# Optimization experiments

Hardware: AMD Instinct MI355X
Metric: run time of the kernel (lower is better)

The kernel has to match this reference:

```python
import math
import jax, jax.numpy as jnp
import numpy as np

C, H, W = 128, 64, 64
R, K = 7, 3          # 7x3 dilated window
PAD_H, PAD_W = 9, 2  # from unfold paddings
DIL_H, DIL_W = 3, 2  # row/col dilations


def _neighborhood(x):
    """Gather dilated 7x3 neighborhood: out[n,c,r,k,i,j] = x[n,c, i+3r-9, j+2k-2] (zero-padded).
    x: (n,c,h,w) -> (n,c,7,3,h,w)."""
    n, c, h, w = x.shape
    xp = jnp.pad(x, ((0, 0), (0, 0), (PAD_H, PAD_H), (PAD_W, PAD_W)))
    taps = [xp[:, :, DIL_H * r:DIL_H * r + h, DIL_W * k:DIL_W * k + w]
            for r in range(R) for k in range(K)]
    return jnp.stack(taps, axis=2).reshape(n, c, R, K, h, w)


def setup_inputs() -> dict:
    key = jax.random.key(0)
    k1, k2, k3 = jax.random.split(key, 3)
    x = jax.random.normal(k1, (4, C, H, W), dtype=jnp.float32)
    p5_w = 0.1 * jax.random.normal(k2, (1, C, R, K, H, W), dtype=jnp.float32)
    p6_w = 0.1 * jax.random.normal(k3, (1, C, R, K, C), dtype=jnp.float32)
    return {"x": x, "p5_w": p5_w, "p6_w": p6_w}


def reference(x, p5_w, p6_w):
    n, c, h, w = x.shape
    # t_2: dilated 7x3 neighborhood gather (double unfold)
    t2 = _neighborhood(x)                                   # (n,c,7,3,h,w)
    # t_3: bmm((n,c*21,hw), (n,hw,c)) / sqrt(hw)
    t3 = jnp.einsum('ncrkhw,ndhw->ncrkd', t2, x) / math.sqrt(h * w)  # (n,c,7,3,c)
    # elementwise modulation
    t7 = p5_w * t2 + t2                                     # (n,c,7,3,h,w)
    t6 = p6_w * t3                                          # (n,c,7,3,c)
    # t_8: bmm((n,hw,c*21), (n,c*21,c)) / sqrt(c*21)
    t8 = jnp.einsum('ncrkhw,ncrkd->nhwd', t7, t6) / math.sqrt(c * R * K)  # (n,h,w,c)
    return jnp.transpose(t8, (0, 3, 1, 2))                  # (n,c,h,w)
```

## Files before the change

### kernel.cpp

```cpp
#include <hip/hip_runtime.h>

typedef _Float16 f16;
typedef _Float16 f16x2 __attribute__((ext_vector_type(2)));
typedef _Float16 f16x4 __attribute__((ext_vector_type(4)));
typedef _Float16 f16x8 __attribute__((ext_vector_type(8)));
typedef float    f32x4 __attribute__((ext_vector_type(4)));

#define XROWS 82
#define XSTR  (XROWS * 64)
#define XK_ELEMS (3u * 4u * 128u * (unsigned)XSTR)
static const size_t T6T_OFF   = (size_t)XK_ELEMS * 2;
static const size_t T6T_BYTES = (size_t)4 * 128 * 2688 * 2;
static const size_t T3P_OFF   = T6T_OFF + T6T_BYTES;
static const size_t T8P_OFF   = T3P_OFF;

__device__ __forceinline__ void gl16(const f16* g, f16* l) {
  __builtin_amdgcn_global_load_lds((const __attribute__((address_space(1))) void*)g,
                                   (__attribute__((address_space(3))) void*)l, 16, 0, 0);
}

__global__ __launch_bounds__(256) void prep_kernel(const float* __restrict__ x,
                                                   f16* __restrict__ xk) {
  unsigned p = blockIdx.x * 256u + threadIdx.x;
  unsigned total = 3u * 4u * 128u * 82u * 32u;
  if (p >= total) return;
  unsigned wp   = p & 31u;
  unsigned row  = (p >> 5) % 82u;
  unsigned rest = p / (32u * 82u);
  unsigned c    = rest & 127u;
  unsigned rest2 = rest >> 7;
  unsigned n    = rest2 & 3u;
  unsigned kc   = rest2 >> 2;
  int hsrc = (int)row - 9;
  int wsrc = (int)(wp * 2u) + 2 * (int)kc - 2;
  f16x2 v; v.x = (f16)0.f; v.y = (f16)0.f;
  if (hsrc >= 0 && hsrc < 64 && wsrc >= 0 && wsrc < 64) {
    const float2* src = (const float2*)(x + (((size_t)(n * 128u + c) * 64u + (unsigned)hsrc) * 64u + (unsigned)wsrc));
    float2 xv = *src;
    v.x = (f16)(xv.x * 0.125f);
    v.y = (f16)(xv.y * 0.125f);
  }
  ((f16x2*)xk)[p] = v;
}

__global__ __launch_bounds__(256, 3) void gram_kernel(const f16* __restrict__ xk,
                                                      f16* __restrict__ t3p) {
  __shared__ f16 gl[2 * 12288];

  unsigned b    = blockIdx.x;
  unsigned ks   = b & 7u;
  unsigned cseg = (b >> 3) & 1u;
  unsigned rki  = (b >> 4) % 11u;
  unsigned n    = b / 176u;
  unsigned r    = rki / 3u;
  unsigned kc   = rki - r * 3u;

  unsigned tid  = threadIdx.x;
  unsigned wv   = tid >> 6;
  unsigned lane = tid & 63u;
  unsigned wy   = wv >> 1;
  unsigned wx   = wv & 1u;
  unsigned quad = lane >> 4;
  unsigned l16  = lane & 15u;
  unsigned rsl  = lane >> 3;
  unsigned seg  = (lane & 7u) ^ (rsl & 7u);

  unsigned h0 = ks * 8u;
  const f16* Ab = xk + (size_t)(kc * 4u + n) * 128u * XSTR + (size_t)(cseg * 64u) * XSTR
                + (h0 + 3u * r) * 64u + seg * 8u;
  const f16* Bb = xk + (size_t)(4u + n) * 128u * XSTR + (h0 + 9u) * 64u + seg * 8u;
  unsigned ar0 = wv * 16u;
  unsigned br0 = wv * 32u;

  f32x4 acc[2][4] = {};

#pragma unroll
  for (unsigned t = 0; t < 2u; t++)
    gl16(Ab + (size_t)(ar0 + t * 8u + rsl) * XSTR, &gl[(ar0 + t * 8u) * 64u]);
#pragma unroll
  for (unsigned t = 0; t < 4u; t++)
    gl16(Bb + (size_t)(br0 + t * 8u + rsl) * XSTR, &gl[4096u + (br0 + t * 8u) * 64u]);

  for (unsigned s = 0; s < 8u; s++) {
    __syncthreads();
    if (s < 7u) {
      f16* base = &gl[((s + 1u) & 1u) * 12288u];
      unsigned off = (s + 1u) * 64u;
#pragma unroll
      for (unsigned t = 0; t < 2u; t++)
        gl16(Ab + off + (size_t)(ar0 + t * 8u + rsl) * XSTR, base + (ar0 + t * 8u) * 64u);
#pragma unroll
      for (unsigned t = 0; t < 4u; t++)
        gl16(Bb + off + (size_t)(br0 + t * 8u + rsl) * XSTR, base + 4096u + (br0 + t * 8u) * 64u);
    }
    const f16* bufA = &gl[(s & 1u) * 12288u];
    const f16* bufB = bufA + 4096u;
#pragma unroll
    for (unsigned t2 = 0; t2 < 2u; t2++) {
      unsigned L = t2 * 4u + quad;
      f16x8 a[2], bb[4];
#pragma unroll
      for (int ms = 0; ms < 2; ms++) {
        unsigned rr = wy * 32u + (unsigned)ms * 16u + l16;
        a[ms] = *(const f16x8*)&bufA[rr * 64u + (L ^ (rr & 7u)) * 8u];
      }
#pragma unroll
      for (int ns = 0; ns < 4; ns++) {
        unsigned rb = wx * 64u + (unsigned)ns * 16u + l16;
        bb[ns] = *(const f16x8*)&bufB[rb * 64u + (L ^ (rb & 7u)) * 8u];
      }
#pragma unroll
      for (int ms = 0; ms < 2; ms++)
#pragma unroll
        for (int ns = 0; ns < 4; ns++)
          acc[ms][ns] = __builtin_amdgcn_mfma_f32_16x16x32_f16(a[ms], bb[ns], acc[ms][ns], 0, 0, 0);
    }
  }

  f16* tp = t3p + ((size_t)(ks * 4u + n) * 11u + rki) * 16384u;
#pragma unroll
  for (int ms = 0; ms < 2; ms++) {
#pragma unroll
    for (int ns = 0; ns < 4; ns++) {
      unsigned c0 = cseg * 64u + wy * 32u + (unsigned)ms * 16u + quad * 4u;
      unsigned d  = wx * 64u + (unsigned)ns * 16u + l16;
#pragma unroll
      for (int reg = 0; reg < 4; reg++)
        tp[(size_t)(c0 + (unsigned)reg) * 128u + d] = (f16)acc[ms][ns][reg];
    }
  }
}

__global__ __launch_bounds__(256) void ep_kernel(const f16* __restrict__ t3p,
                                                 const float* __restrict__ p6,
                                                 f16* __restrict__ t6T) {
  unsigned idx = blockIdx.x * 256u + threadIdx.x;
  unsigned t   = idx >> 12;
  unsigned rk  = t % 21u;
  unsigned n   = t / 21u;

  if (rk <= 10u) {
    unsigned d4 = idx & 31u;
    unsigned c  = (idx >> 5) & 127u;
    unsigned d0 = d4 * 4u;
    float s0 = 0.f, s1 = 0.f, s2 = 0.f, s3 = 0.f;
#pragma unroll
    for (unsigned ks = 0; ks < 8u; ks++) {
      f16x4 v = *(const f16x4*)(t3p + (((size_t)(ks * 4u + n) * 11u + rk) * 16384u + c * 128u + d0));
      s0 += (float)v[0]; s1 += (float)v[1]; s2 += (float)v[2]; s3 += (float)v[3];
    }
    const float* pp = p6 + ((size_t)c * 21u + rk) * 128u + d0;
    f16* ob = t6T + (size_t)(n * 128u + d0) * 2688u + rk * 128u + c;
    ob[0]        = (f16)(s0 * pp[0]);
    ob[2688]     = (f16)(s1 * pp[1]);
    ob[2 * 2688] = (f16)(s2 * pp[2]);
    ob[3 * 2688] = (f16)(s3 * pp[3]);
  } else {
    unsigned mrk = 20u - rk;
    unsigned c4 = idx & 31u;
    unsigned d  = (idx >> 5) & 127u;
    unsigned c0 = c4 * 4u;
    float s0 = 0.f, s1 = 0.f, s2 = 0.f, s3 = 0.f;
#pragma unroll
    for (unsigned ks = 0; ks < 8u; ks++) {
      f16x4 v = *(const f16x4*)(t3p + (((size_t)(ks * 4u + n) * 11u + mrk) * 16384u + d * 128u + c0));
      s0 += (float)v[0]; s1 += (float)v[1]; s2 += (float)v[2]; s3 += (float)v[3];
    }
    f16x4 o;
    o[0] = (f16)(s0 * p6[((size_t)(c0 + 0u) * 21u + rk) * 128u + d]);
    o[1] = (f16)(s1 * p6[((size_t)(c0 + 1u) * 21u + rk) * 128u + d]);
    o[2] = (f16)(s2 * p6[((size_t)(c0 + 2u) * 21u + rk) * 128u + d]);
    o[3] = (f16)(s3 * p6[((size_t)(c0 + 3u) * 21u + rk) * 128u + d]);
    *(f16x4*)(t6T + (size_t)(n * 128u + d) * 2688u + rk * 128u + c0) = o;
  }
}

#define ALDS_STR 40
#define RT_STR   66
__global__ __launch_bounds__(256, 4) void outp_kernel(const f16* __restrict__ xk,
                                                      const float* __restrict__ p5,
                                                      const f16* __restrict__ t6T,
                                                      f16* __restrict__ t8p) {
  __shared__ float smem[8448];
  f16* Alds = (f16*)smem;

  unsigned b = blockIdx.x;
  unsigned g = b & 3u;
  unsigned h = (b >> 2) & 63u;
  unsigned n = b >> 8;

  unsigned tid  = threadIdx.x;
  unsigned wv   = tid >> 6;
  unsigned lane = tid & 63u;
  unsigned wy   = wv >> 1;
  unsigned wx   = wv & 1u;
  unsigned quad = lane >> 4;
  unsigned l16  = lane & 15u;
  unsigned wst  = tid & 63u;
  unsigned g8   = tid >> 6;

  unsigned cbase = g * 32u + g8 * 8u;
  const float* prow0 = p5 + (size_t)cbase * (21u * 4096u) + h * 64u + wst;
  const f16* bfb = t6T + (size_t)(n * 128u + wx * 64u + l16) * 2688u + g * 32u + quad * 8u;

  f32x4 acc[2][4] = {};
  f16 xv[8]; float pv[8];
  f16x8 bfc[4];

  {
    const f16* xrow = xk + (((size_t)n * 128u + cbase) * XROWS + h) * 64u + wst;
#pragma unroll
    for (int i = 0; i < 8; i++) { xv[i] = xrow[(size_t)i * XSTR]; pv[i] = prow0[(size_t)i * (21u * 4096u)]; }
#pragma unroll
    for (int ns = 0; ns < 4; ns++) bfc[ns] = *(const f16x8*)(bfb + (size_t)ns * 16u * 2688u);
  }

  for (unsigned j = 0; j < 21u; j++) {
    f16* Ag = Alds + (j & 1u) * 2560u;
    {
      f16x8 av;
#pragma unroll
      for (int i = 0; i < 8; i++) av[i] = (f16)((float)xv[i] * (1.0f + pv[i]));
      *(f16x8*)&Ag[wst * ALDS_STR + g8 * 8u] = av;
    }
    __syncthreads();

    f16x8 bfn[4];
    if (j < 20u) {
      unsigned rk = j + 1u;
      unsigned rr = rk / 3u;
      unsigned kcc = rk - rr * 3u;
      const f16* xrow = xk + (((size_t)(kcc * 4u + n) * 128u + cbase) * XROWS + (h + 3u * rr)) * 64u + wst;
      const float* prow = prow0 + rk * 4096u;
#pragma unroll
      for (int i = 0; i < 8; i++) { xv[i] = xrow[(size_t)i * XSTR]; pv[i] = prow[(size_t)i * (21u * 4096u)]; }
#pragma unroll
      for (int ns = 0; ns < 4; ns++) bfn[ns] = *(const f16x8*)(bfb + (size_t)ns * 16u * 2688u + rk * 128u);
    }

    f16x8 a[2];
#pragma unroll
    for (int ms = 0; ms < 2; ms++)
      a[ms] = *(const f16x8*)&Ag[(wy * 32u + (unsigned)ms * 16u + l16) * ALDS_STR + quad * 8u];
#pragma unroll
    for (int ms = 0; ms < 2; ms++)
#pragma unroll
      for (int ns = 0; ns < 4; ns++)
        acc[ms][ns] = __builtin_amdgcn_mfma_f32_16x16x32_f16(a[ms], bfc[ns], acc[ms][ns], 0, 0, 0);
#pragma unroll
    for (int ns = 0; ns < 4; ns++) bfc[ns] = bfn[ns];
  }

  __syncthreads();
  float* Rt = smem;
#pragma unroll
  for (int ms = 0; ms < 2; ms++)
#pragma unroll
    for (int ns = 0; ns < 4; ns++) {
      unsigned w0 = wy * 32u + (unsigned)ms * 16u + quad * 4u;
      unsigned d  = wx * 64u + (unsigned)ns * 16u + l16;
#pragma unroll
      for (int reg = 0; reg < 4; reg++)
        Rt[d * RT_STR + w0 + (unsigned)reg] = acc[ms][ns][reg];
    }
  __syncthreads();
  f16* op = t8p + ((size_t)((g * 4u + n) * 64u + h)) * 8192u;
#pragma unroll
  for (unsigned it = 0; it < 4u; it++) {
    unsigned row = (tid >> 3) + it * 32u;
    unsigned w0  = (tid & 7u) * 8u;
    f16x8 o;
#pragma unroll
    for (int i = 0; i < 8; i++) o[i] = (f16)Rt[row * RT_STR + w0 + (unsigned)i];
    *(f16x8*)(op + row * 64u + w0) = o;
  }
}

__global__ __launch_bounds__(256) void red_kernel(const f16* __restrict__ t8p,
                                                  float* __restrict__ out) {
  unsigned idx = blockIdx.x * 256u + threadIdx.x;
  unsigned w0 = (idx & 7u) * 8u;
  unsigned h  = (idx >> 3) & 63u;
  unsigned d  = (idx >> 9) & 127u;
  unsigned n  = idx >> 16;
  const float FS = 0.15430334996209192f;
  float s[8] = {};
#pragma unroll
  for (unsigned g = 0; g < 4u; g++) {
    f16x8 v = *(const f16x8*)(t8p + ((size_t)((g * 4u + n) * 64u + h)) * 8192u + d * 64u + w0);
#pragma unroll
    for (int i = 0; i < 8; i++) s[i] += (float)v[i];
  }
  f32x4 o0, o1;
#pragma unroll
  for (int i = 0; i < 4; i++) { o0[i] = s[i] * FS; o1[i] = s[i + 4] * FS; }
  float* op = out + ((size_t)(n * 128u + d) * 64u + h) * 64u + w0;
  *(f32x4*)op = o0;
  *(f32x4*)(op + 4) = o1;
}

extern "C" void kernel_launch(void* const* d_in, const int* in_sizes, int n_in,
                              void* d_out, int out_size, void* d_ws, size_t ws_size,
                              hipStream_t stream) {
  const float* x  = (const float*)d_in[0];
  const float* p5 = (const float*)d_in[1];
  const float* p6 = (const float*)d_in[2];
  float* out = (float*)d_out;
  f16* xk  = (f16*)((char*)d_ws);
  f16* t6T = (f16*)((char*)d_ws + T6T_OFF);
  f16* t3p = (f16*)((char*)d_ws + T3P_OFF);
  f16* t8p = (f16*)((char*)d_ws + T8P_OFF);

  unsigned prep_blocks = (3u * 4u * 128u * 82u * 32u + 255u) / 256u;
  hipLaunchKernelGGL(prep_kernel, dim3(prep_blocks), dim3(256), 0, stream, x, xk);
  hipLaunchKernelGGL(gram_kernel, dim3(704),  dim3(256), 0, stream, xk, t3p);
  hipLaunchKernelGGL(ep_kernel,   dim3(1344), dim3(256), 0, stream, t3p, p6, t6T);
  hipLaunchKernelGGL(outp_kernel, dim3(1024), dim3(256), 0, stream, xk, p5, t6T, t8p);
  hipLaunchKernelGGL(red_kernel,  dim3(1024), dim3(256), 0, stream, t8p, out);
}
```

Baseline: 167.0 us.

## Store t6 in MFMA-fragment blocked layout and double outp threads per block

The epilogue now writes t6 in a blocked layout that matches the MFMA B-fragment order, so each lane of outp_kernel loads its fragment as one contiguous 16-byte read instead of a strided row access. outp_kernel moves to 512 threads arranged as 2x4 waves. Each wave owns a 32x32 output tile and each thread builds 4 channels of the A tile instead of 8. This cuts per-thread registers and load latency and raises the wave count per block. The cost is more waves contending at each barrier and narrower LDS writes.

Result: faster. 149.3 us (-10.6%).

```diff
diff --git a/kernel.cpp b/kernel.cpp
--- a/kernel.cpp
+++ b/kernel.cpp
@@ -133,11 +133,12 @@
 
 __global__ __launch_bounds__(256) void ep_kernel(const f16* __restrict__ t3p,
                                                  const float* __restrict__ p6,
-                                                 f16* __restrict__ t6T) {
+                                                 f16* __restrict__ t6B) {
   unsigned idx = blockIdx.x * 256u + threadIdx.x;
   unsigned t   = idx >> 12;
   unsigned rk  = t % 21u;
   unsigned n   = t / 21u;
+  f16* tb = t6B + (size_t)t * 16384u;
 
   if (rk <= 10u) {
     unsigned d4 = idx & 31u;
@@ -150,11 +151,11 @@
       s0 += (float)v[0]; s1 += (float)v[1]; s2 += (float)v[2]; s3 += (float)v[3];
     }
     const float* pp = p6 + ((size_t)c * 21u + rk) * 128u + d0;
-    f16* ob = t6T + (size_t)(n * 128u + d0) * 2688u + rk * 128u + c;
-    ob[0]        = (f16)(s0 * pp[0]);
-    ob[2688]     = (f16)(s1 * pp[1]);
-    ob[2 * 2688] = (f16)(s2 * pp[2]);
-    ob[3 * 2688] = (f16)(s3 * pp[3]);
+    f16* ob = tb + (c >> 5) * 4096u + (d0 >> 4) * 512u + ((c >> 3) & 3u) * 128u + (d0 & 15u) * 8u + (c & 7u);
+    ob[0]  = (f16)(s0 * pp[0]);
+    ob[8]  = (f16)(s1 * pp[1]);
+    ob[16] = (f16)(s2 * pp[2]);
+    ob[24] = (f16)(s3 * pp[3]);
   } else {
     unsigned mrk = 20u - rk;
     unsigned c4 = idx & 31u;
@@ -171,15 +172,15 @@
     o[1] = (f16)(s1 * p6[((size_t)(c0 + 1u) * 21u + rk) * 128u + d]);
     o[2] = (f16)(s2 * p6[((size_t)(c0 + 2u) * 21u + rk) * 128u + d]);
     o[3] = (f16)(s3 * p6[((size_t)(c0 + 3u) * 21u + rk) * 128u + d]);
-    *(f16x4*)(t6T + (size_t)(n * 128u + d) * 2688u + rk * 128u + c0) = o;
+    *(f16x4*)(tb + (c0 >> 5) * 4096u + (d >> 4) * 512u + ((c0 >> 3) & 3u) * 128u + (d & 15u) * 8u + (c0 & 7u)) = o;
   }
 }
 
 #define ALDS_STR 40
 #define RT_STR   66
-__global__ __launch_bounds__(256, 4) void outp_kernel(const f16* __restrict__ xk,
+__global__ __launch_bounds__(512, 8) void outp_kernel(const f16* __restrict__ xk,
                                                       const float* __restrict__ p5,
-                                                      const f16* __restrict__ t6T,
+                                                      const f16* __restrict__ t6B,
                                                       f16* __restrict__ t8p) {
   __shared__ float smem[8448];
   f16* Alds = (f16*)smem;
@@ -192,50 +193,50 @@
   unsigned tid  = threadIdx.x;
   unsigned wv   = tid >> 6;
   unsigned lane = tid & 63u;
-  unsigned wy   = wv >> 1;
-  unsigned wx   = wv & 1u;
+  unsigned wy   = wv >> 2;
+  unsigned wx   = wv & 3u;
   unsigned quad = lane >> 4;
   unsigned l16  = lane & 15u;
   unsigned wst  = tid & 63u;
   unsigned g8   = tid >> 6;
-
-  unsigned cbase = g * 32u + g8 * 8u;
-  const float* prow0 = p5 + (size_t)cbase * (21u * 4096u) + h * 64u + wst;
-  const f16* bfb = t6T + (size_t)(n * 128u + wx * 64u + l16) * 2688u + g * 32u + quad * 8u;
-
-  f32x4 acc[2][4] = {};
-  f16 xv[8]; float pv[8];
-  f16x8 bfc[4];
+  unsigned cth  = g * 32u + g8 * 4u;
+
+  const float* prow0 = p5 + (size_t)cth * (21u * 4096u) + h * 64u + wst;
+  const f16* t6b = t6B + (size_t)n * 344064u + g * 4096u + (size_t)lane * 8u;
+
+  f32x4 acc[2][2] = {};
+  f16 xv[4]; float pv[4];
+  f16x8 bfc[2];
 
   {
-    const f16* xrow = xk + (((size_t)n * 128u + cbase) * XROWS + h) * 64u + wst;
-#pragma unroll
-    for (int i = 0; i < 8; i++) { xv[i] = xrow[(size_t)i * XSTR]; pv[i] = prow0[(size_t)i * (21u * 4096u)]; }
-#pragma unroll
-    for (int ns = 0; ns < 4; ns++) bfc[ns] = *(const f16x8*)(bfb + (size_t)ns * 16u * 2688u);
+    const f16* xrow = xk + (((size_t)n * 128u + cth) * XROWS + h) * 64u + wst;
+#pragma unroll
+    for (int i = 0; i < 4; i++) { xv[i] = xrow[(size_t)i * XSTR]; pv[i] = prow0[(size_t)i * (21u * 4096u)]; }
+#pragma unroll
+    for (int ns = 0; ns < 2; ns++) bfc[ns] = *(const f16x8*)(t6b + (wx * 2u + (unsigned)ns) * 512u);
   }
 
   for (unsigned j = 0; j < 21u; j++) {
     f16* Ag = Alds + (j & 1u) * 2560u;
     {
-      f16x8 av;
-#pragma unroll
-      for (int i = 0; i < 8; i++) av[i] = (f16)((float)xv[i] * (1.0f + pv[i]));
-      *(f16x8*)&Ag[wst * ALDS_STR + g8 * 8u] = av;
+      f16x4 av;
+#pragma unroll
+      for (int i = 0; i < 4; i++) av[i] = (f16)((float)xv[i] * (1.0f + pv[i]));
+      *(f16x4*)&Ag[wst * ALDS_STR + g8 * 4u] = av;
     }
     __syncthreads();
 
-    f16x8 bfn[4];
+    f16x8 bfn[2];
     if (j < 20u) {
       unsigned rk = j + 1u;
       unsigned rr = rk / 3u;
       unsigned kcc = rk - rr * 3u;
-      const f16* xrow = xk + (((size_t)(kcc * 4u + n) * 128u + cbase) * XROWS + (h + 3u * rr)) * 64u + wst;
+      const f16* xrow = xk + (((size_t)(kcc * 4u + n) * 128u + cth) * XROWS + (h + 3u * rr)) * 64u + wst;
       const float* prow = prow0 + rk * 4096u;
 #pragma unroll
-      for (int i = 0; i < 8; i++) { xv[i] = xrow[(size_t)i * XSTR]; pv[i] = prow[(size_t)i * (21u * 4096u)]; }
-#pragma unroll
-      for (int ns = 0; ns < 4; ns++) bfn[ns] = *(const f16x8*)(bfb + (size_t)ns * 16u * 2688u + rk * 128u);
+      for (int i = 0; i < 4; i++) { xv[i] = xrow[(size_t)i * XSTR]; pv[i] = prow[(size_t)i * (21u * 4096u)]; }
+#pragma unroll
+      for (int ns = 0; ns < 2; ns++) bfn[ns] = *(const f16x8*)(t6b + rk * 16384u + (wx * 2u + (unsigned)ns) * 512u);
     }
 
     f16x8 a[2];
@@ -245,10 +246,10 @@
 #pragma unroll
     for (int ms = 0; ms < 2; ms++)
 #pragma unroll
-      for (int ns = 0; ns < 4; ns++)
+      for (int ns = 0; ns < 2; ns++)
         acc[ms][ns] = __builtin_amdgcn_mfma_f32_16x16x32_f16(a[ms], bfc[ns], acc[ms][ns], 0, 0, 0);
 #pragma unroll
-    for (int ns = 0; ns < 4; ns++) bfc[ns] = bfn[ns];
+    for (int ns = 0; ns < 2; ns++) bfc[ns] = bfn[ns];
   }
 
   __syncthreads();
@@ -256,23 +257,26 @@
 #pragma unroll
   for (int ms = 0; ms < 2; ms++)
 #pragma unroll
-    for (int ns = 0; ns < 4; ns++) {
+    for (int ns = 0; ns < 2; ns++) {
       unsigned w0 = wy * 32u + (unsigned)ms * 16u + quad * 4u;
-      unsigned d  = wx * 64u + (unsigned)ns * 16u + l16;
+      unsigned d  = wx * 32u + (unsigned)ns * 16u + l16;
 #pragma unroll
       for (int reg = 0; reg < 4; reg++)
         Rt[d * RT_STR + w0 + (unsigned)reg] = acc[ms][ns][reg];
     }
   __syncthreads();
   f16* op = t8p + ((size_t)((g * 4u + n) * 64u + h)) * 8192u;
-#pragma unroll
-  for (unsigned it = 0; it < 4u; it++) {
-    unsigned row = (tid >> 3) + it * 32u;
-    unsigned w0  = (tid & 7u) * 8u;
-    f16x8 o;
-#pragma unroll
-    for (int i = 0; i < 8; i++) o[i] = (f16)Rt[row * RT_STR + w0 + (unsigned)i];
-    *(f16x8*)(op + row * 64u + w0) = o;
+  {
+    unsigned row = tid >> 2;
+    unsigned w0  = (tid & 3u) * 16u;
+    f16x8 o0, o1;
+#pragma unroll
+    for (int i = 0; i < 8; i++) {
+      o0[i] = (f16)Rt[row * RT_STR + w0 + (unsigned)i];
+      o1[i] = (f16)Rt[row * RT_STR + w0 + 8u + (unsigned)i];
+    }
+    *(f16x8*)(op + row * 64u + w0) = o0;
+    *(f16x8*)(op + row * 64u + w0 + 8u) = o1;
   }
 }
 
@@ -307,14 +311,14 @@
   const float* p6 = (const float*)d_in[2];
   float* out = (float*)d_out;
   f16* xk  = (f16*)((char*)d_ws);
-  f16* t6T = (f16*)((char*)d_ws + T6T_OFF);
+  f16* t6B = (f16*)((char*)d_ws + T6T_OFF);
   f16* t3p = (f16*)((char*)d_ws + T3P_OFF);
   f16* t8p = (f16*)((char*)d_ws + T8P_OFF);
 
   unsigned prep_blocks = (3u * 4u * 128u * 82u * 32u + 255u) / 256u;
   hipLaunchKernelGGL(prep_kernel, dim3(prep_blocks), dim3(256), 0, stream, x, xk);
   hipLaunchKernelGGL(gram_kernel, dim3(704),  dim3(256), 0, stream, xk, t3p);
-  hipLaunchKernelGGL(ep_kernel,   dim3(1344), dim3(256), 0, stream, t3p, p6, t6T);
-  hipLaunchKernelGGL(outp_kernel, dim3(1024), dim3(256), 0, stream, xk, p5, t6T, t8p);
+  hipLaunchKernelGGL(ep_kernel,   dim3(1344), dim3(256), 0, stream, t3p, p6, t6B);
+  hipLaunchKernelGGL(outp_kernel, dim3(1024), dim3(512), 0, stream, xk, p5, t6B, t8p);
   hipLaunchKernelGGL(red_kernel,  dim3(1024), dim3(256), 0, stream, t8p, out);
 }
```
